# Kernel optimization log

Hardware: AMD Instinct MI355X
Metric: run time of the kernel (lower is better)

Reference implementation:

```python
import jax, jax.numpy as jnp
import numpy as np
import math

B, N, C, H = 32, 512, 768, 12
HD = C // H
KEEP_RATE = 0.7
SCALE = HD ** -0.5
BOUNDARY = math.ceil(KEEP_RATE * (N - 1))  # 358


def setup_inputs() -> dict:
    key = jax.random.key(0)
    k1, k2, k3, k4 = jax.random.split(key, 4)
    x = jax.random.normal(k1, (B, N, C), jnp.float32) * 0.02
    # prefix (left-aligned) key-padding mask: valid length per sample in [N//4, N]
    lengths = jax.random.randint(k2, (B,), N // 4, N + 1)
    key_mask = (jnp.arange(N)[None, :] < lengths[:, None])  # [B, N]
    attn_mask = jnp.broadcast_to(key_mask[:, None, :], (B, N, N)).astype(jnp.int32)
    w_qkv = jax.random.normal(k3, (C, 3 * C), jnp.float32) * (C ** -0.5)
    w_proj = jax.random.normal(k4, (C, C), jnp.float32) * (C ** -0.5)
    b_proj = jnp.zeros((C,), jnp.float32)
    return {"x": x, "attn_mask": attn_mask, "w_qkv": w_qkv, "w_proj": w_proj, "b_proj": b_proj}


def reference(x, attn_mask, w_qkv, w_proj, b_proj):
    # qkv projection and head split: [B,N,3C] -> [3,B,H,N,HD]
    qkv = (x @ w_qkv).reshape(B, N, 3, H, HD).transpose(2, 0, 3, 1, 4)
    q, k, v = qkv[0], qkv[1], qkv[2]
    attn = jnp.einsum('bhqd,bhkd->bhqk', q, k) * SCALE          # [B,H,N,N]
    mask4 = attn_mask[:, None, :, :]                            # broadcast over heads
    attn = jnp.where(mask4 == 0, jnp.float32(-1e9), attn)
    attn = jax.nn.softmax(attn, axis=-1)
    out = jnp.einsum('bhqk,bhkd->bhqd', attn, v)                # [B,H,N,HD]
    out = out.transpose(0, 2, 1, 3).reshape(B, N, C)
    out = out @ w_proj + b_proj

    # per-sample top-k token pruning based on CLS attention (keep_rate < 1)
    key_row = attn_mask[:, 0, 1:]                               # [B, N-1] key padding row
    cls_mean = attn[:, :, 0, 1:].mean(axis=1)                   # mean over heads, [B, N-1]
    valid = key_row != 0
    scores = jnp.where(valid, cls_mean, -jnp.inf)
    valid_count = valid.sum(axis=1)                             # [B]
    left = jnp.ceil(valid_count.astype(jnp.float32) * KEEP_RATE).astype(jnp.int32)
    _, top_idx = jax.lax.top_k(scores, BOUNDARY)                # sorted desc, [B, BOUNDARY]
    pos = jnp.arange(BOUNDARY)[None, :]
    # slots beyond per-sample left_tokens are padded with 1e9 (matches torch cat padding)
    idx = jnp.where(pos < left[:, None], top_idx.astype(jnp.float32), jnp.float32(1e9))
    index = jnp.broadcast_to(idx[:, :, None], (B, BOUNDARY, C))
    return (out, index, idx, BOUNDARY)
```

## Files before the change

kernel.cpp:

```cpp
#include <hip/hip_runtime.h>
#include <hip/hip_bf16.h>

#define Bb 32
#define Nn 512
#define Cc 768
#define Hh 12
#define HDd 64
#define BND 358
#define QS 0.18033688f

typedef unsigned short u16;
typedef unsigned int u32;
typedef __attribute__((ext_vector_type(8))) short bf16x8;
typedef __attribute__((ext_vector_type(4))) float f32x4;
typedef __attribute__((ext_vector_type(16))) float f32x16;
typedef __attribute__((ext_vector_type(4))) int i32x4;

__device__ __forceinline__ f32x4 MFMA16(bf16x8 a, bf16x8 b, f32x4 c) {
  return __builtin_amdgcn_mfma_f32_16x16x32_bf16(a, b, c, 0, 0, 0);
}
__device__ __forceinline__ f32x16 MFMA32(bf16x8 a, bf16x8 b, f32x16 c) {
  return __builtin_amdgcn_mfma_f32_32x32x16_bf16(a, b, c, 0, 0, 0);
}

__device__ __forceinline__ u32 f2bf(float f) {
  u32 u = __builtin_bit_cast(u32, f);
  return (u + 0x7fffu + ((u >> 16) & 1u)) >> 16;
}
__device__ __forceinline__ u32 packbf2(float a, float b) { return f2bf(a) | (f2bf(b) << 16); }
__device__ __forceinline__ u32 cvtpk2(float a, float b) {
  float2 f2 = {a, b};
  __hip_bfloat162 h = __float22bfloat162_rn(f2);
  u32 r;
  __builtin_memcpy(&r, &h, 4);
  return r;
}
__device__ __forceinline__ float bf2f(u16 h) { return __builtin_bit_cast(float, (u32)h << 16); }

__device__ __forceinline__ void async_copy16(void* lds, const void* g) {
  __builtin_amdgcn_global_load_lds((const __attribute__((address_space(1))) void*)g,
                                   (__attribute__((address_space(3))) void*)lds, 16, 0, 0);
}


__global__ __launch_bounds__(256) void k_convx(const float* __restrict__ x, u16* __restrict__ xb) {
  int gid = blockIdx.x * 256 + threadIdx.x;
  if (gid >= (Bb * Nn * Cc) / 4) return;
  float4 v = *(const float4*)&x[gid * 4];
  u32 p0 = packbf2(v.x, v.y), p1 = packbf2(v.z, v.w);
  uint2 st = {p0, p1};
  *(uint2*)&xb[gid * 4] = st;
}

__global__ __launch_bounds__(256) void k_transpose(const float* __restrict__ src, u16* __restrict__ dst,
                                                   int R, int Ccols) {
  __shared__ float tbuf[32][33];
  int c0 = blockIdx.x * 32, r0 = blockIdx.y * 32;
  int lx = threadIdx.x & 31, ly = threadIdx.x >> 5;
  #pragma unroll
  for (int rr = ly; rr < 32; rr += 8) tbuf[rr][lx] = src[(long)(r0 + rr) * Ccols + c0 + lx];
  __syncthreads();
  #pragma unroll
  for (int cc = ly; cc < 32; cc += 8) dst[(long)(c0 + cc) * R + r0 + lx] = (u16)f2bf(tbuf[lx][cc]);
}

__global__ __launch_bounds__(256) void k_lens(const int* __restrict__ mask, int* __restrict__ lens) {
  int b = blockIdx.x, t = threadIdx.x;
  __shared__ int red[256];
  red[t] = mask[(long)b * Nn * Nn + t] + mask[(long)b * Nn * Nn + t + 256];
  __syncthreads();
  for (int s = 128; s > 0; s >>= 1) {
    if (t < s) red[t] += red[t + s];
    __syncthreads();
  }
  if (t == 0) lens[b] = red[0];
}

template <int MODE, int SWAP>
__global__ __launch_bounds__(256) void k_gemm2(const u16* __restrict__ A, const u16* __restrict__ Bt,
                                               int nb0, u16* __restrict__ Qo, u16* __restrict__ Ko,
                                               u16* __restrict__ Vto, float* __restrict__ Co,
                                               const float* __restrict__ bias) {
  __shared__ u16 As[2][128 * 64];
  __shared__ u16 Bs[2][128 * 64];
  int m0 = blockIdx.x * 128;
  int nb = nb0 + blockIdx.y * 128;
  int t = threadIdx.x, lane = t & 63, wave = t >> 6;
  int wr = wave >> 1, wc = wave & 1;
  int qlane = lane & 15, g = lane >> 4;
  f32x4 acc[4][4] = {};

  auto stage = [&](int kt, int buf) {
    #pragma unroll
    for (int i = 0; i < 4; ++i) {
      int chunk = i * 256 + t;
      int row = chunk >> 3;
      int cp = (chunk & 7) << 4;
      int src = cp ^ ((row & 7) << 4);
      const u16* ga = A + (long)(m0 + row) * 768 + kt * 64 + (src >> 1);
      const u16* gb = Bt + (long)(nb + row) * 768 + kt * 64 + (src >> 1);
      async_copy16(&As[buf][(i * 256 + wave * 64) * 8], ga);
      async_copy16(&Bs[buf][(i * 256 + wave * 64) * 8], gb);
    }
  };

  auto compute = [&](int buf) {
    #pragma unroll
    for (int kk = 0; kk < 2; ++kk) {
      bf16x8 af[4], bf[4];
      #pragma unroll
      for (int x = 0; x < 4; ++x) {
        int ra = wr * 64 + x * 16 + qlane;
        int ca = (kk * 64 + g * 16) ^ ((ra & 7) << 4);
        af[x] = *(const bf16x8*)&As[buf][ra * 64 + (ca >> 1)];
        int rb = wc * 64 + x * 16 + qlane;
        int cb = (kk * 64 + g * 16) ^ ((rb & 7) << 4);
        bf[x] = *(const bf16x8*)&Bs[buf][rb * 64 + (cb >> 1)];
      }
      #pragma unroll
      for (int mi = 0; mi < 4; ++mi)
        #pragma unroll
        for (int ni = 0; ni < 4; ++ni)
          acc[mi][ni] = SWAP ? MFMA16(bf[ni], af[mi], acc[mi][ni])
                             : MFMA16(af[mi], bf[ni], acc[mi][ni]);
    }
  };

  stage(0, 0);
  __syncthreads();
  int cur = 0;
  for (int kt = 0; kt < 12; ++kt) {
    if (kt < 11) stage(kt + 1, cur ^ 1);
    compute(cur);
    __syncthreads();
    cur ^= 1;
  }

  if (MODE == 0 && SWAP == 1) {
    #pragma unroll
    for (int mi = 0; mi < 4; ++mi) {
      int m = m0 + wr * 64 + mi * 16 + qlane;
      int b = m >> 9, qi = m & 511;
      #pragma unroll
      for (int ni = 0; ni < 4; ++ni) {
        int nf = nb + wc * 64 + ni * 16 + g * 4;
        int which = nf >= 768;
        int rem = nf - which * 768;
        int hh = rem >> 6, d0 = rem & 63;
        u16* dst = (which ? Ko : Qo) + ((long)(b * Hh + hh) * Nn + qi) * HDd + d0;
        float sc = which ? 1.f : QS;
        uint2 st = {packbf2(acc[mi][ni][0] * sc, acc[mi][ni][1] * sc),
                    packbf2(acc[mi][ni][2] * sc, acc[mi][ni][3] * sc)};
        *(uint2*)dst = st;
      }
    }
  } else if (MODE == 0) {
    #pragma unroll
    for (int mi = 0; mi < 4; ++mi) {
      int m = m0 + wr * 64 + mi * 16 + g * 4;
      int b = m >> 9, qi = m & 511;
      #pragma unroll
      for (int ni = 0; ni < 4; ++ni) {
        int rem = nb + wc * 64 + ni * 16 + qlane - 1536;
        int hh = rem >> 6, d = rem & 63;
        u16* dst = Vto + ((long)(b * Hh + hh) * HDd + d) * Nn + qi;
        uint2 st = {packbf2(acc[mi][ni][0], acc[mi][ni][1]),
                    packbf2(acc[mi][ni][2], acc[mi][ni][3])};
        *(uint2*)dst = st;
      }
    }
  } else {
    #pragma unroll
    for (int mi = 0; mi < 4; ++mi) {
      #pragma unroll
      for (int ni = 0; ni < 4; ++ni) {
        int n = nb + wc * 64 + ni * 16 + qlane;
        float bv = bias[n];
        #pragma unroll
        for (int r = 0; r < 4; ++r) {
          int m = m0 + wr * 64 + mi * 16 + g * 4 + r;
          Co[(long)m * Cc + n] = acc[mi][ni][r] + bv;
        }
      }
    }
  }
}

__global__ __launch_bounds__(256) void k_attn(const u16* __restrict__ Q, const u16* __restrict__ K,
                                              const u16* __restrict__ Vt, const int* __restrict__ lens,
                                              u16* __restrict__ AO) {
  int wave = threadIdx.x >> 6, lane = threadIdx.x & 63;
  int bid = blockIdx.x;
  int half = bid & 1, h = (bid >> 1) % Hh, b = bid / (2 * Hh);
  int q0w = half * 256 + wave * 64;
  int ln = lane & 31, hi = lane >> 5;
  int len = lens[b];
  int nt = (len + 31) >> 5;

  const u16* Qb = Q + (long)(b * Hh + h) * Nn * HDd;
  const u16* Kb = K + (long)(b * Hh + h) * Nn * HDd;
  const u16* Vb = Vt + (long)(b * Hh + h) * HDd * Nn;

  bf16x8 qf[2][4];
  #pragma unroll
  for (int qt = 0; qt < 2; ++qt)
    #pragma unroll
    for (int ds = 0; ds < 4; ++ds)
      qf[qt][ds] = *(const bf16x8*)(Qb + (q0w + qt * 32 + ln) * HDd + ds * 16 + hi * 8);

  f32x16 o[2][2] = {};
  float l[2] = {0.f, 0.f};

  #pragma unroll 1
  for (int t = 0; t < nt; ++t) {
    int k0 = t * 32;
    bf16x8 kf[4], vf[2][2];
    #pragma unroll
    for (int ds = 0; ds < 4; ++ds)
      kf[ds] = *(const bf16x8*)(Kb + (k0 + ln) * HDd + ds * 16 + hi * 8);
    #pragma unroll
    for (int dt = 0; dt < 2; ++dt)
      #pragma unroll
      for (int ks = 0; ks < 2; ++ks)
        vf[dt][ks] = *(const bf16x8*)(Vb + (dt * 32 + ln) * Nn + k0 + ks * 16 + hi * 8);

    bool bdry = (k0 + 32 > len);
    int khi = k0 + 4 * hi;

    #pragma unroll
    for (int qt = 0; qt < 2; ++qt) {
      f32x16 st = {};
      #pragma unroll
      for (int ds = 0; ds < 4; ++ds) st = MFMA32(kf[ds], qf[qt][ds], st);
      if (bdry) {
        #pragma unroll
        for (int r = 0; r < 16; ++r) {
          int key = khi + (r & 3) + 8 * (r >> 2);
          if (key >= len) st[r] = -1e9f;
        }
      }
      float p[16];
      #pragma unroll
      for (int r = 0; r < 16; ++r) p[r] = exp2f(st[r]);
      l[qt] += (((p[0] + p[1]) + (p[2] + p[3])) + ((p[4] + p[5]) + (p[6] + p[7]))) +
               (((p[8] + p[9]) + (p[10] + p[11])) + ((p[12] + p[13]) + (p[14] + p[15])));
      u32 wA0 = cvtpk2(p[0], p[1]), wA1 = cvtpk2(p[2], p[3]);
      u32 wA2 = cvtpk2(p[4], p[5]), wA3 = cvtpk2(p[6], p[7]);
      asm volatile("v_permlane32_swap_b32 %0, %1" : "+v"(wA0), "+v"(wA2));
      asm volatile("v_permlane32_swap_b32 %0, %1" : "+v"(wA1), "+v"(wA3));
      u32 wB0 = cvtpk2(p[8], p[9]), wB1 = cvtpk2(p[10], p[11]);
      u32 wB2 = cvtpk2(p[12], p[13]), wB3 = cvtpk2(p[14], p[15]);
      asm volatile("v_permlane32_swap_b32 %0, %1" : "+v"(wB0), "+v"(wB2));
      asm volatile("v_permlane32_swap_b32 %0, %1" : "+v"(wB1), "+v"(wB3));
      i32x4 bi0 = {(int)wA0, (int)wA1, (int)wA2, (int)wA3};
      i32x4 bi1 = {(int)wB0, (int)wB1, (int)wB2, (int)wB3};
      bf16x8 pb0 = __builtin_bit_cast(bf16x8, bi0);
      bf16x8 pb1 = __builtin_bit_cast(bf16x8, bi1);
      #pragma unroll
      for (int dt = 0; dt < 2; ++dt) {
        o[qt][dt] = MFMA32(vf[dt][0], pb0, o[qt][dt]);
        o[qt][dt] = MFMA32(vf[dt][1], pb1, o[qt][dt]);
      }
    }
  }

  #pragma unroll
  for (int qt = 0; qt < 2; ++qt) {
    float ls = l[qt] + __shfl_xor(l[qt], 32);
    float inv = 1.f / ls;
    u16* outp = AO + ((long)(b * Nn + q0w + qt * 32 + ln) * Cc) + h * HDd;
    #pragma unroll
    for (int dt = 0; dt < 2; ++dt) {
      #pragma unroll
      for (int qd = 0; qd < 4; ++qd) {
        uint2 st2 = {cvtpk2(o[qt][dt][4 * qd + 0] * inv, o[qt][dt][4 * qd + 1] * inv),
                     cvtpk2(o[qt][dt][4 * qd + 2] * inv, o[qt][dt][4 * qd + 3] * inv)};
        *(uint2*)(outp + dt * 32 + 8 * qd + 4 * hi) = st2;
      }
    }
  }
}

__global__ __launch_bounds__(256) void k_sco_init(float* __restrict__ sco) {
  int gid = blockIdx.x * 256 + threadIdx.x;
  if (gid < Bb * 511) sco[gid] = 0.f;
}

__global__ __launch_bounds__(256) void k_cls(const u16* __restrict__ Q, const u16* __restrict__ K,
                                             const int* __restrict__ lens, float* __restrict__ scores) {
  int bh = blockIdx.x;
  int b = bh / Hh;
  int t = threadIdx.x;
  int len = lens[b];
  __shared__ float qrow[64];
  __shared__ float red[256];
  const u16* Qb = Q + (long)bh * Nn * HDd;
  const u16* Kb = K + (long)bh * Nn * HDd;
  if (t < 64) qrow[t] = bf2f(Qb[t]);
  __syncthreads();
  const bf16x8* kr0 = (const bf16x8*)(Kb + t * HDd);
  const bf16x8* kr1 = (const bf16x8*)(Kb + (t + 256) * HDd);
  float d0 = 0.f, d1 = 0.f;
  #pragma unroll
  for (int c8 = 0; c8 < 8; ++c8) {
    bf16x8 kv0 = kr0[c8], kv1 = kr1[c8];
    #pragma unroll
    for (int j = 0; j < 8; ++j) {
      float qv = qrow[c8 * 8 + j];
      d0 += qv * bf2f((u16)kv0[j]);
      d1 += qv * bf2f((u16)kv1[j]);
    }
  }
  float l0 = (t < len) ? d0 : -1e9f;
  float l1 = (t + 256 < len) ? d1 : -1e9f;
  red[t] = fmaxf(l0, l1);
  __syncthreads();
  for (int ss = 128; ss > 0; ss >>= 1) {
    if (t < ss) red[t] = fmaxf(red[t], red[t + ss]);
    __syncthreads();
  }
  float mx = red[0];
  __syncthreads();
  float e0 = exp2f(l0 - mx), e1 = exp2f(l1 - mx);
  red[t] = e0 + e1;
  __syncthreads();
  for (int ss = 128; ss > 0; ss >>= 1) {
    if (t < ss) red[t] += red[t + ss];
    __syncthreads();
  }
  float w = (1.f / 12.f) / red[0];
  if (t >= 1) atomicAdd(&scores[b * 511 + (t - 1)], e0 * w);
  atomicAdd(&scores[b * 511 + (t + 255)], e1 * w);
}

__device__ __forceinline__ bool sless(float sa, int ia, float sb, int ib) {
  return (sa > sb) || (sa == sb && ia < ib);
}

__global__ __launch_bounds__(256) void k_topk(const float* __restrict__ scores,
                                              const int* __restrict__ lens, float* __restrict__ dout) {
  int b = blockIdx.x, t = threadIdx.x;
  __shared__ float sc[512];
  __shared__ int id[512];
  float ninf = -__builtin_inff();
  int len = lens[b];
  for (int i = t; i < 512; i += 256) {
    sc[i] = (i < 511 && (i + 1) < len) ? scores[b * 511 + i] : ninf;
    id[i] = i;
  }
  for (int k = 2; k <= 512; k <<= 1) {
    for (int j = k >> 1; j > 0; j >>= 1) {
      __syncthreads();
      for (int i = t; i < 512; i += 256) {
        int ixj = i ^ j;
        if (ixj > i) {
          float si = sc[i], sj = sc[ixj];
          int ii = id[i], ij = id[ixj];
          bool up = ((i & k) == 0);
          bool dosw = up ? sless(sj, ij, si, ii) : sless(si, ii, sj, ij);
          if (dosw) {
            sc[i] = sj; sc[ixj] = si;
            id[i] = ij; id[ixj] = ii;
          }
        }
      }
    }
  }
  __syncthreads();
  int left = (int)ceilf((float)(len - 1) * 0.7f);
  const long OFF_IDX = (long)Bb * Nn * Cc + (long)Bb * BND * Cc;
  for (int p = t; p < BND; p += 256) {
    dout[OFF_IDX + (long)b * BND + p] = (p < left) ? (float)id[p] : 1e9f;
  }
  if (b == 0 && t == 0) dout[OFF_IDX + (long)Bb * BND] = (float)BND;
}

__global__ __launch_bounds__(256) void k_bcast(float* __restrict__ dout) {
  long gid = (long)blockIdx.x * 256 + threadIdx.x;
  const long total = (long)Bb * BND * (Cc / 4);
  if (gid >= total) return;
  long bp = gid / (Cc / 4);
  int c4 = (int)(gid % (Cc / 4));
  const long OFF_INDEX = (long)Bb * Nn * Cc;
  const long OFF_IDX = OFF_INDEX + (long)Bb * BND * Cc;
  float v = dout[OFF_IDX + bp];
  float4 f = {v, v, v, v};
  *(float4*)&dout[OFF_INDEX + bp * Cc + (long)c4 * 4] = f;
}

extern "C" void kernel_launch(void* const* d_in, const int* in_sizes, int n_in,
                              void* d_out, int out_size, void* d_ws, size_t ws_size,
                              hipStream_t stream) {
  const float* x = (const float*)d_in[0];
  const int* mask = (const int*)d_in[1];
  const float* wqkv = (const float*)d_in[2];
  const float* wproj = (const float*)d_in[3];
  const float* bproj = (const float*)d_in[4];
  float* out = (float*)d_out;

  char* ws = (char*)d_ws;
  u16* Qw  = (u16*)(ws);
  u16* Kw  = (u16*)(ws + 25165824L);
  u16* Vtw = (u16*)(ws + 50331648L);
  u16* XB  = (u16*)(ws + 75497472L);
  u16* AO  = XB;
  u16* WQT = (u16*)(ws + 100663296L);
  u16* WPT = (u16*)(ws + 104202240L);
  float* SCO = (float*)(ws + 105381888L);
  int* LEN = (int*)(ws + 105447424L);

  k_convx<<<12288, 256, 0, stream>>>(x, XB);
  k_transpose<<<dim3(72, 24), 256, 0, stream>>>(wqkv, WQT, 768, 2304);
  k_transpose<<<dim3(24, 24), 256, 0, stream>>>(wproj, WPT, 768, 768);
  k_lens<<<32, 256, 0, stream>>>(mask, LEN);
  k_sco_init<<<64, 256, 0, stream>>>(SCO);
  k_gemm2<0, 1><<<dim3(128, 12), 256, 0, stream>>>(XB, WQT, 0, Qw, Kw, nullptr, nullptr, nullptr);
  k_gemm2<0, 0><<<dim3(128, 6), 256, 0, stream>>>(XB, WQT, 1536, nullptr, nullptr, Vtw, nullptr, nullptr);
  k_attn<<<768, 256, 0, stream>>>(Qw, Kw, Vtw, LEN, AO);
  k_gemm2<1, 0><<<dim3(128, 6), 256, 0, stream>>>(AO, WPT, 0, nullptr, nullptr, nullptr, out, bproj);
  k_cls<<<384, 256, 0, stream>>>(Qw, Kw, LEN, SCO);
  k_topk<<<32, 256, 0, stream>>>(SCO, LEN, out);
  k_bcast<<<8592, 256, 0, stream>>>(out);
}
```

Baseline: 236.1 us.

## Stage K/V tiles in double-buffered swizzled LDS via async copies

The attention kernel now cooperatively loads 64-key K and V tiles into double-buffered, XOR-swizzled shared memory with async 16-byte copies, prefetching the next tile while computing on the current one. The QKV GEMM epilogue writes V in a key-blocked layout (32-key by 64-dim chunks) so each staged tile is contiguous. This is meant to stop the four waves in a block from each fetching the same K/V from global memory, and to hide load latency. In exchange it adds a barrier per tile and uses LDS, which may lower occupancy. Correctness depends on the async copies completing before the barrier.

```diff
diff --git a/kernel.cpp b/kernel.cpp
--- a/kernel.cpp
+++ b/kernel.cpp
@@ -163,7 +163,7 @@
       for (int ni = 0; ni < 4; ++ni) {
         int rem = nb + wc * 64 + ni * 16 + qlane - 1536;
         int hh = rem >> 6, d = rem & 63;
-        u16* dst = Vto + ((long)(b * Hh + hh) * HDd + d) * Nn + qi;
+        u16* dst = Vto + (long)(b * Hh + hh) * (Nn * HDd) + (qi >> 5) * 2048 + d * 32 + (qi & 31);
         uint2 st = {packbf2(acc[mi][ni][0], acc[mi][ni][1]),
                     packbf2(acc[mi][ni][2], acc[mi][ni][3])};
         *(uint2*)dst = st;
@@ -189,17 +189,38 @@
 __global__ __launch_bounds__(256) void k_attn(const u16* __restrict__ Q, const u16* __restrict__ K,
                                               const u16* __restrict__ Vt, const int* __restrict__ lens,
                                               u16* __restrict__ AO) {
-  int wave = threadIdx.x >> 6, lane = threadIdx.x & 63;
+  int tid = threadIdx.x;
+  int wave = tid >> 6, lane = tid & 63;
   int bid = blockIdx.x;
   int half = bid & 1, h = (bid >> 1) % Hh, b = bid / (2 * Hh);
   int q0w = half * 256 + wave * 64;
   int ln = lane & 31, hi = lane >> 5;
   int len = lens[b];
-  int nt = (len + 31) >> 5;
+  int nt = (len + 63) >> 6;
 
   const u16* Qb = Q + (long)(b * Hh + h) * Nn * HDd;
   const u16* Kb = K + (long)(b * Hh + h) * Nn * HDd;
-  const u16* Vb = Vt + (long)(b * Hh + h) * HDd * Nn;
+  const u16* Vb = Vt + (long)(b * Hh + h) * Nn * HDd;
+
+  __shared__ u16 Kl[2][4096];
+  __shared__ u16 Vl[2][4096];
+
+  auto stage = [&](int t, int buf) {
+    const char* ksrc = (const char*)(Kb + (long)t * 64 * HDd);
+    const char* vsrc = (const char*)(Vb + (long)t * 64 * HDd);
+    #pragma unroll
+    for (int i = 0; i < 2; ++i) {
+      int d0 = i * 4096 + tid * 16;
+      int rk = d0 >> 7;
+      int gk = d0 ^ ((rk & 7) << 4);
+      int dv = (d0 >> 6) & 63;
+      int gv = d0 ^ ((((dv >> 1) & 1) << 5) | (((dv >> 2) & 1) << 4));
+      char* kdst = (char*)(&Kl[0][0]) + buf * 8192 + i * 4096 + wave * 1024;
+      char* vdst = (char*)(&Vl[0][0]) + buf * 8192 + i * 4096 + wave * 1024;
+      async_copy16(kdst, ksrc + gk);
+      async_copy16(vdst, vsrc + gv);
+    }
+  };
 
   bf16x8 qf[2][4];
   #pragma unroll
@@ -211,21 +232,25 @@
   f32x16 o[2][2] = {};
   float l[2] = {0.f, 0.f};
 
-  #pragma unroll 1
-  for (int t = 0; t < nt; ++t) {
-    int k0 = t * 32;
+  auto subtile = [&](int buf, int ks2, int k0s) {
     bf16x8 kf[4], vf[2][2];
     #pragma unroll
-    for (int ds = 0; ds < 4; ++ds)
-      kf[ds] = *(const bf16x8*)(Kb + (k0 + ln) * HDd + ds * 16 + hi * 8);
+    for (int ds = 0; ds < 4; ++ds) {
+      int row = ks2 * 32 + ln;
+      int c = (ds * 32 + hi * 16) ^ ((row & 7) << 4);
+      kf[ds] = *(const bf16x8*)((const char*)(&Kl[0][0]) + buf * 8192 + row * 128 + c);
+    }
     #pragma unroll
     for (int dt = 0; dt < 2; ++dt)
       #pragma unroll
-      for (int ks = 0; ks < 2; ++ks)
-        vf[dt][ks] = *(const bf16x8*)(Vb + (dt * 32 + ln) * Nn + k0 + ks * 16 + hi * 8);
-
-    bool bdry = (k0 + 32 > len);
-    int khi = k0 + 4 * hi;
+      for (int ks = 0; ks < 2; ++ks) {
+        int d = dt * 32 + ln;
+        int c = (ks * 32 + hi * 16) ^ ((((d >> 1) & 1) << 5) | (((d >> 2) & 1) << 4));
+        vf[dt][ks] = *(const bf16x8*)((const char*)(&Vl[0][0]) + buf * 8192 + ks2 * 4096 + d * 64 + c);
+      }
+
+    bool bdry = (k0s + 32 > len);
+    int khi = k0s + 4 * hi;
 
     #pragma unroll
     for (int qt = 0; qt < 2; ++qt) {
@@ -262,6 +287,17 @@
         o[qt][dt] = MFMA32(vf[dt][1], pb1, o[qt][dt]);
       }
     }
+  };
+
+  stage(0, 0);
+  __syncthreads();
+  #pragma unroll 1
+  for (int t = 0; t < nt; ++t) {
+    if (t + 1 < nt) stage(t + 1, (t + 1) & 1);
+    int buf = t & 1, k0 = t * 64;
+    subtile(buf, 0, k0);
+    if (k0 + 32 < len) subtile(buf, 1, k0 + 32);
+    __syncthreads();
   }
 
   #pragma unroll
```

Result: no change. 234.5 us (-0.7%).
